# Performance work log

Measured on AMD Instinct MI355X. Metric: run time of the kernel, lower is better.

Reference implementation:

```python
import jax, jax.numpy as jnp
import numpy as np

N = 50000        # nodes
E = 800000       # edges
D_IN = 512       # input_shape
PROJ = 256       # proj_dim
H = 4            # num_heads
C = 32           # hidden_channels
HC = H * C
NUM_LABELS = 10
SLOPE = 0.2      # GATv2 LeakyReLU negative slope


def _glorot(key, shape):
    fan_in = shape[-1]
    return jax.random.normal(key, shape, jnp.float32) / jnp.sqrt(jnp.float32(fan_in))


def setup_inputs() -> dict:
    key = jax.random.key(0)
    ks = jax.random.split(key, 16)
    inp = {}
    inp["x"] = jax.random.normal(ks[0], (N, D_IN), jnp.float32)
    inp["edge_index"] = jax.random.randint(ks[1], (2, E), 0, N, dtype=jnp.int64)
    # projection Linear
    inp["W_proj"] = _glorot(ks[2], (PROJ, D_IN)); inp["b_proj"] = jnp.zeros((PROJ,), jnp.float32)
    # GATv2 layer 1: lin_l, lin_r, att, bias
    inp["Wl1"] = _glorot(ks[3], (HC, PROJ)); inp["bl1"] = jnp.zeros((HC,), jnp.float32)
    inp["Wr1"] = _glorot(ks[4], (HC, PROJ)); inp["br1"] = jnp.zeros((HC,), jnp.float32)
    inp["att1"] = _glorot(ks[5], (H, C)); inp["bias1"] = jnp.zeros((HC,), jnp.float32)
    # GATv2 layer 2
    inp["Wl2"] = _glorot(ks[6], (HC, HC)); inp["bl2"] = jnp.zeros((HC,), jnp.float32)
    inp["Wr2"] = _glorot(ks[7], (HC, HC)); inp["br2"] = jnp.zeros((HC,), jnp.float32)
    inp["att2"] = _glorot(ks[8], (H, C)); inp["bias2"] = jnp.zeros((HC,), jnp.float32)
    # head MLP
    inp["W1"] = _glorot(ks[9], (C, HC)); inp["b1"] = jnp.zeros((C,), jnp.float32)
    inp["W2"] = _glorot(ks[10], (NUM_LABELS, C)); inp["b2"] = jnp.zeros((NUM_LABELS,), jnp.float32)
    return inp


def _gatv2(x, src, dst, Wl, bl, Wr, br, att, bias):
    # x: [N, F_in]; src/dst: [E]. PyG GATv2Conv, concat=True, no self-loops, eval (no dropout).
    xl = (x @ Wl.T + bl).reshape(N, H, C)   # source transform
    xr = (x @ Wr.T + br).reshape(N, H, C)   # target transform
    e = jax.nn.leaky_relu(xl[src] + xr[dst], negative_slope=SLOPE)  # [E,H,C]
    logit = jnp.einsum('ehc,hc->eh', e, att)                        # [E,H]
    # segment softmax over incoming edges of each destination node
    m = jax.ops.segment_max(logit, dst, num_segments=N)             # [N,H]
    m = jnp.where(jnp.isfinite(m), m, jnp.float32(0))               # empty segments -> 0
    p = jnp.exp(logit - m[dst])                                     # [E,H]
    s = jax.ops.segment_sum(p, dst, num_segments=N)                 # [N,H]
    alpha = p / (s[dst] + jnp.float32(1e-16))                       # [E,H]
    out = jax.ops.segment_sum(xl[src] * alpha[:, :, None], dst, num_segments=N)  # [N,H,C]
    return out.reshape(N, HC) + bias


def reference(x, edge_index, W_proj, b_proj, Wl1, bl1, Wr1, br1, att1, bias1,
              Wl2, bl2, Wr2, br2, att2, bias2, W1, b1, W2, b2):
    src, dst = edge_index[0], edge_index[1]
    h = jax.nn.elu(x @ W_proj.T + b_proj)
    h = jax.nn.elu(_gatv2(h, src, dst, Wl1, bl1, Wr1, br1, att1, bias1))
    h = jax.nn.elu(_gatv2(h, src, dst, Wl2, bl2, Wr2, br2, att2, bias2))
    h = jax.nn.elu(h @ W1.T + b1)
    return h @ W2.T + b2
```

## Files before the change

kernel.cpp:

```cpp
#include <hip/hip_runtime.h>
#include <cstdint>
#include <cstddef>

constexpr int NN = 50000;
constexpr int NE = 800000;

typedef _Float16 half8 __attribute__((ext_vector_type(8)));
typedef _Float16 half4v __attribute__((ext_vector_type(4)));
typedef _Float16 half2v __attribute__((ext_vector_type(2)));
typedef float f32x16 __attribute__((ext_vector_type(16)));
typedef unsigned short ushort_t;

__device__ inline ushort_t f2h(float f) {
  _Float16 h = (_Float16)f;
  return __builtin_bit_cast(ushort_t, h);
}

#if __has_builtin(__builtin_amdgcn_fdot2)
__device__ inline float fdot2(half2v a, half2v b, float c) {
  return __builtin_amdgcn_fdot2(a, b, c, false);
}
#else
__device__ inline float fdot2(half2v a, half2v b, float c) {
  return c + (float)a[0] * (float)b[0] + (float)a[1] * (float)b[1];
}
#endif

__global__ void k_wconv(const float* __restrict__ W, ushort_t* __restrict__ Bh,
                        int M, int K, int total) {
  int idx = blockIdx.x * 256 + threadIdx.x;
  if (idx >= total) return;
  int j = idx & 7;
  int l = (idx >> 3) & 63;
  int blk = idx >> 9;
  int nKB = K >> 4;
  int cb = blk / nKB, kb = blk - cb * nKB;
  int col = cb * 32 + (l & 31);
  int k = kb * 16 + ((l >> 5) & 1) * 8 + j;
  float v = (col < M) ? W[(size_t)col * K + k] : 0.f;
  Bh[idx] = f2h(v);
}

__global__ __launch_bounds__(512) void gemm_proj_l1(const float* __restrict__ x,
    const ushort_t* __restrict__ WpF, const ushort_t* __restrict__ WB1,
    const float* __restrict__ bp, const float* __restrict__ bl1,
    const float* __restrict__ br1, ushort_t* __restrict__ xlh,
    ushort_t* __restrict__ xrh, int N)
{
  constexpr int NKK = 4;
  constexpr int nKB1 = 32;
  constexpr int nK1 = 8;
  __shared__ ushort_t Ah[2][2 * NKK * 512];
  __shared__ ushort_t H0[16384];
  const int t = threadIdx.x;
  const int lane = t & 63;
  const int wid = t >> 6;
  const int wr = wid >> 2;
  const int wc = wid & 3;
  const int row0 = blockIdx.x * 64;
  const int cb0 = wc * 2;

  const int s_r = t >> 4, s_k = (t & 15) * 4;
  const int sb0 = (s_k >> 4) * 512 + (s_r + 32 * ((s_k >> 3) & 1)) * 8 + (s_k & 7);
  const int sb1 = sb0 + NKK * 512;
  const bool ok0 = (row0 + s_r) < N;
  const bool ok1 = (row0 + s_r + 32) < N;
  const float* ap0 = x + (size_t)(row0 + s_r) * 512 + s_k;
  const float* ap1 = x + (size_t)(row0 + s_r + 32) * 512 + s_k;

  f32x16 acc0 = {}, acc1 = {};
  float4 f0 = make_float4(0, 0, 0, 0), f1 = make_float4(0, 0, 0, 0);

  auto aload = [&](int ks) {
    f0 = make_float4(0, 0, 0, 0);
    f1 = make_float4(0, 0, 0, 0);
    if (ok0) f0 = *(const float4*)(ap0 + (size_t)ks * 64);
    if (ok1) f1 = *(const float4*)(ap1 + (size_t)ks * 64);
  };
  auto cvt4 = [](float4 f) {
    half4v h;
    h[0] = (_Float16)f.x; h[1] = (_Float16)f.y;
    h[2] = (_Float16)f.z; h[3] = (_Float16)f.w;
    return h;
  };
  auto stage_write = [&](int buf) {
    *(half4v*)&Ah[buf][sb0] = cvt4(f0);
    *(half4v*)&Ah[buf][sb1] = cvt4(f1);
  };

  aload(0);
  stage_write(0);
  __syncthreads();

  for (int ks = 0; ks < nK1; ++ks) {
    const int cur = ks & 1;
    const int nxt = cur ^ 1;
    const bool have_next = (ks + 1 < nK1);
    if (have_next) aload(ks + 1);

    #pragma unroll
    for (int kk = 0; kk < NKK; ++kk) {
      const int kbg = ks * NKK + kk;
      half8 ah = *(const half8*)&Ah[cur][(wr * NKK + kk) * 512 + lane * 8];
      const size_t bo0 = ((size_t)(cb0 * nKB1 + kbg) * 64 + lane) * 8;
      half8 bh0 = *(const half8*)(WpF + bo0);
      acc0 = __builtin_amdgcn_mfma_f32_32x32x16_f16(ah, bh0, acc0, 0, 0, 0);
      const size_t bo1 = ((size_t)((cb0 + 1) * nKB1 + kbg) * 64 + lane) * 8;
      half8 bh1 = *(const half8*)(WpF + bo1);
      acc1 = __builtin_amdgcn_mfma_f32_32x32x16_f16(ah, bh1, acc1, 0, 0, 0);
    }

    if (have_next) stage_write(nxt);
    __syncthreads();
  }

  {
    int col = cb0 * 32 + (lane & 31);
    float bv = bp[col];
    #pragma unroll
    for (int r = 0; r < 16; ++r) {
      int row = wr * 32 + (r & 3) + 8 * (r >> 2) + 4 * (lane >> 5);
      float v = acc0[r] + bv;
      v = v > 0.f ? v : (__expf(v) - 1.f);
      H0[((row >> 5) * 16 + (col >> 4)) * 512 +
         ((row & 31) + 32 * ((col >> 3) & 1)) * 8 + (col & 7)] = f2h(v);
    }
    int col1 = col + 32;
    float bv1 = bp[col1];
    #pragma unroll
    for (int r = 0; r < 16; ++r) {
      int row = wr * 32 + (r & 3) + 8 * (r >> 2) + 4 * (lane >> 5);
      float v = acc1[r] + bv1;
      v = v > 0.f ? v : (__expf(v) - 1.f);
      H0[((row >> 5) * 16 + (col1 >> 4)) * 512 +
         ((row & 31) + 32 * ((col1 >> 3) & 1)) * 8 + (col1 & 7)] = f2h(v);
    }
  }
  __syncthreads();

  f32x16 acc2a = {}, acc2b = {};
  #pragma unroll
  for (int kk = 0; kk < 16; ++kk) {
    half8 ah = *(const half8*)&H0[(wr * 16 + kk) * 512 + lane * 8];
    const size_t bo0 = ((size_t)(cb0 * 16 + kk) * 64 + lane) * 8;
    half8 bh0 = *(const half8*)(WB1 + bo0);
    acc2a = __builtin_amdgcn_mfma_f32_32x32x16_f16(ah, bh0, acc2a, 0, 0, 0);
    const size_t bo1 = ((size_t)((cb0 + 1) * 16 + kk) * 64 + lane) * 8;
    half8 bh1 = *(const half8*)(WB1 + bo1);
    acc2b = __builtin_amdgcn_mfma_f32_32x32x16_f16(ah, bh1, acc2b, 0, 0, 0);
  }

  auto epi2 = [&](const f32x16& acc, int cb) {
    int cc = cb * 32 + (lane & 31);
    float bv = (cc < 128) ? bl1[cc] : br1[cc - 128];
    #pragma unroll
    for (int r = 0; r < 16; ++r) {
      int rr = row0 + wr * 32 + (r & 3) + 8 * (r >> 2) + 4 * (lane >> 5);
      if (rr < N) {
        float v = acc[r] + bv;
        if (cc < 128) xlh[(size_t)rr * 128 + cc] = f2h(v);
        else          xrh[(size_t)rr * 128 + (cc - 128)] = f2h(v);
      }
    }
  };
  epi2(acc2a, cb0);
  epi2(acc2b, cb0 + 1);
}

template<int ACT, int OUTMODE, int BKT, int AFP16, int NCB>
__global__ __launch_bounds__(512) void gemm_mfma(const void* __restrict__ Av,
    const ushort_t* __restrict__ Bh,
    const float* __restrict__ bias, const float* __restrict__ bias2,
    float* __restrict__ C, ushort_t* __restrict__ C16a,
    ushort_t* __restrict__ C16b, int N, int M, int K)
{
  constexpr int NKK = BKT / 16;
  __shared__ ushort_t Ah[2][2 * NKK * 512];
  const int t = threadIdx.x;
  const int lane = t & 63;
  const int wid = t >> 6;
  const int wr = wid >> 2;
  const int wc = wid & 3;
  const int row0 = blockIdx.x * 64;
  const int col0 = blockIdx.y * (128 * NCB);
  const int nKB = K >> 4;
  const int nK = K / BKT;
  const int cb0 = (col0 >> 5) + wc * NCB;

  int s_r, s_k, sb0, sb1 = 0;
  bool ok0 = false, ok1 = false;
  if constexpr (!AFP16) {
    s_r = t >> 4; s_k = (t & 15) * 4;
    sb0 = (s_k >> 4) * 512 + (s_r + 32 * ((s_k >> 3) & 1)) * 8 + (s_k & 7);
    sb1 = sb0 + NKK * 512;
    ok0 = (row0 + s_r) < N;
    ok1 = (row0 + s_r + 32) < N;
  } else if constexpr (BKT == 64) {
    s_r = t >> 3; s_k = (t & 7) * 8;
    sb0 = ((s_r >> 5) * NKK + (s_k >> 4)) * 512 +
          ((s_r & 31) + 32 * ((s_k >> 3) & 1)) * 8;
    ok0 = (row0 + s_r) < N;
  } else {
    s_r = t >> 3; s_k = (t & 7) * 4;
    sb0 = ((s_r >> 5) * NKK + (s_k >> 4)) * 512 +
          ((s_r & 31) + 32 * ((s_k >> 3) & 1)) * 8 + (s_k & 7);
    ok0 = (row0 + s_r) < N;
  }
  const float*    ap0 = (const float*)Av + (size_t)(row0 + s_r) * K + s_k;
  const float*    ap1 = (const float*)Av + (size_t)(row0 + s_r + 32) * K + s_k;
  const ushort_t* aph = (const ushort_t*)Av + (size_t)(row0 + s_r) * K + s_k;

  f32x16 acc0 = {}, acc1 = {};
  float4 f0 = make_float4(0, 0, 0, 0), f1 = make_float4(0, 0, 0, 0);
  half8 h8 = {};
  half4v h4 = {};

  auto aload = [&](int ks) {
    if constexpr (!AFP16) {
      f0 = make_float4(0, 0, 0, 0);
      f1 = make_float4(0, 0, 0, 0);
      if (ok0) f0 = *(const float4*)(ap0 + (size_t)ks * BKT);
      if (ok1) f1 = *(const float4*)(ap1 + (size_t)ks * BKT);
    } else if constexpr (BKT == 64) {
      half8 z = {};
      h8 = ok0 ? *(const half8*)(aph + (size_t)ks * BKT) : z;
    } else {
      half4v z = {};
      h4 = ok0 ? *(const half4v*)(aph + (size_t)ks * BKT) : z;
    }
  };
  auto cvt4 = [](float4 f) {
    half4v h;
    h[0] = (_Float16)f.x; h[1] = (_Float16)f.y;
    h[2] = (_Float16)f.z; h[3] = (_Float16)f.w;
    return h;
  };
  auto stage_write = [&](int buf) {
    if constexpr (!AFP16) {
      *(half4v*)&Ah[buf][sb0] = cvt4(f0);
      *(half4v*)&Ah[buf][sb1] = cvt4(f1);
    } else if constexpr (BKT == 64) {
      *(half8*)&Ah[buf][sb0] = h8;
    } else {
      *(half4v*)&Ah[buf][sb0] = h4;
    }
  };

  aload(0);
  stage_write(0);
  __syncthreads();

  for (int ks = 0; ks < nK; ++ks) {
    const int cur = ks & 1;
    const int nxt = cur ^ 1;
    const bool have_next = (ks + 1 < nK);
    if (have_next) aload(ks + 1);

    #pragma unroll
    for (int kk = 0; kk < NKK; ++kk) {
      const int kbg = ks * NKK + kk;
      half8 ah = *(const half8*)&Ah[cur][(wr * NKK + kk) * 512 + lane * 8];
      const size_t bo0 = ((size_t)(cb0 * nKB + kbg) * 64 + lane) * 8;
      half8 bh0 = *(const half8*)(Bh + bo0);
      acc0 = __builtin_amdgcn_mfma_f32_32x32x16_f16(ah, bh0, acc0, 0, 0, 0);
      if constexpr (NCB == 2) {
        const size_t bo1 = ((size_t)((cb0 + 1) * nKB + kbg) * 64 + lane) * 8;
        half8 bh1 = *(const half8*)(Bh + bo1);
        acc1 = __builtin_amdgcn_mfma_f32_32x32x16_f16(ah, bh1, acc1, 0, 0, 0);
      }
    }

    if (have_next) stage_write(nxt);
    __syncthreads();
  }

  auto epi = [&](const f32x16& acc, int cb) {
    int cc = cb * 32 + (lane & 31);
    float bv;
    if constexpr (OUTMODE == 3) bv = (cc < 128) ? bias[cc] : bias2[cc - 128];
    else                        bv = (cc < M) ? bias[cc] : 0.f;
    #pragma unroll
    for (int r = 0; r < 16; ++r) {
      int rr = row0 + wr * 32 + (r & 3) + 8 * (r >> 2) + 4 * (lane >> 5);
      if (rr < N && cc < M) {
        float v = acc[r] + bv;
        if (ACT) v = v > 0.f ? v : (__expf(v) - 1.f);
        if constexpr (OUTMODE == 0)      C[(size_t)rr * M + cc] = v;
        else if constexpr (OUTMODE == 1) C16a[(size_t)rr * M + cc] = f2h(v);
        else {
          if (cc < 128) C16a[(size_t)rr * 128 + cc] = f2h(v);
          else          C16b[(size_t)rr * 128 + (cc - 128)] = f2h(v);
        }
      }
    }
  };
  epi(acc0, cb0);
  if constexpr (NCB == 2) epi(acc1, cb0 + 1);
}

__global__ void k_degrank(const int* __restrict__ ei, int* __restrict__ deg,
                          int* __restrict__ rank) {
  int e = blockIdx.x * 256 + threadIdx.x;
  if (e >= NE) return;
  int d = ei[NE + e];
  rank[e] = atomicAdd(&deg[d], 1);
}

__global__ __launch_bounds__(256) void k_scan1(const int* __restrict__ deg,
    int* __restrict__ rowstart, int* __restrict__ blocksum) {
  __shared__ int sm[256];
  int b = blockIdx.x, t = threadIdx.x;
  int i = b * 256 + t;
  int v = (i < NN) ? deg[i] : 0;
  sm[t] = v;
  __syncthreads();
  #pragma unroll
  for (int off = 1; off < 256; off <<= 1) {
    int u = (t >= off) ? sm[t - off] : 0;
    __syncthreads();
    sm[t] += u;
    __syncthreads();
  }
  if (i < NN) rowstart[i + 1] = sm[t];
  if (t == 255) blocksum[b] = sm[255];
}

__global__ __launch_bounds__(256) void k_scan2(int* __restrict__ blocksum, int nb) {
  __shared__ int sm[256];
  int t = threadIdx.x;
  int v = (t < nb) ? blocksum[t] : 0;
  sm[t] = v;
  __syncthreads();
  #pragma unroll
  for (int off = 1; off < 256; off <<= 1) {
    int u = (t >= off) ? sm[t - off] : 0;
    __syncthreads();
    sm[t] += u;
    __syncthreads();
  }
  if (t < nb) blocksum[t] = (t == 0) ? 0 : sm[t - 1];
}

__global__ __launch_bounds__(256) void k_scan3(int* __restrict__ rowstart,
    const int* __restrict__ blocksum) {
  int b = blockIdx.x, t = threadIdx.x;
  int i = b * 256 + t;
  if (i == 0) rowstart[0] = 0;
  if (i < NN) rowstart[i + 1] += blocksum[b];
}

__global__ void k_scatter(const int* __restrict__ ei, const int* __restrict__ rowstart,
                          const int* __restrict__ rank, int* __restrict__ srcp) {
  int e = blockIdx.x * 256 + threadIdx.x;
  if (e >= NE) return;
  int d = ei[NE + e];
  srcp[rowstart[d] + rank[e]] = ei[e];
}

__global__ __launch_bounds__(256) void k_gat(const ushort_t* __restrict__ xl,
    const ushort_t* __restrict__ xr, const int* __restrict__ srcp,
    const int* __restrict__ rowstart, const float* __restrict__ att,
    const float* __restrict__ bias, ushort_t* __restrict__ out)
{
  const int g = threadIdx.x >> 5;
  const int c = threadIdx.x & 31;
  const int n = blockIdx.x * 8 + g;
  const int r0 = rowstart[n], r1 = rowstart[n + 1];
  half4v xrh = *(const half4v*)(xr + (size_t)n * 128 + 4 * c);
  const half2v xr01 = {xrh[0], xrh[1]};
  const half2v xr23 = {xrh[2], xrh[3]};
  const float4 atv = *(const float4*)(att + 4 * c);
  const half2v at01 = {(_Float16)atv.x, (_Float16)atv.y};
  const half2v at23 = {(_Float16)atv.z, (_Float16)atv.w};
  const half2v k02 = {(_Float16)0.2f, (_Float16)0.2f};

  float m = -1e30f, ssum = 0.f;
  float a0 = 0.f, a1 = 0.f, a2 = 0.f, a3 = 0.f;

  auto lg = [&](int s, float4& xs) -> float {
    half4v hv = *(const half4v*)(xl + (size_t)s * 128 + 4 * c);
    xs.x = (float)hv[0]; xs.y = (float)hv[1];
    xs.z = (float)hv[2]; xs.w = (float)hv[3];
    half2v u01 = half2v{hv[0], hv[1]} + xr01;
    half2v u23 = half2v{hv[2], hv[3]} + xr23;
    u01 = __builtin_elementwise_max(u01, u01 * k02);
    u23 = __builtin_elementwise_max(u23, u23 * k02);
    float l = fdot2(u01, at01, fdot2(u23, at23, 0.f));
    l += __shfl_xor(l, 1);
    l += __shfl_xor(l, 2);
    l += __shfl_xor(l, 4);
    return l;
  };

  int j = r0;
  for (; j + 8 <= r1; j += 8) {
    int s0 = srcp[j],     s1 = srcp[j + 1], s2 = srcp[j + 2], s3 = srcp[j + 3];
    int s4 = srcp[j + 4], s5 = srcp[j + 5], s6 = srcp[j + 6], s7 = srcp[j + 7];
    float4 x0, x1, x2, x3, x4, x5, x6, x7;
    float l0 = lg(s0, x0), l1 = lg(s1, x1), l2 = lg(s2, x2), l3 = lg(s3, x3);
    float l4 = lg(s4, x4), l5 = lg(s5, x5), l6 = lg(s6, x6), l7 = lg(s7, x7);
    float mloc = fmaxf(fmaxf(fmaxf(l0, l1), fmaxf(l2, l3)),
                       fmaxf(fmaxf(l4, l5), fmaxf(l6, l7)));
    float mn = fmaxf(m, mloc);
    float sc = __expf(m - mn);
    float p0 = __expf(l0 - mn), p1 = __expf(l1 - mn);
    float p2 = __expf(l2 - mn), p3 = __expf(l3 - mn);
    float p4 = __expf(l4 - mn), p5 = __expf(l5 - mn);
    float p6 = __expf(l6 - mn), p7 = __expf(l7 - mn);
    ssum = ssum * sc + (((p0 + p1) + (p2 + p3)) + ((p4 + p5) + (p6 + p7)));
    a0 = a0 * sc + (((p0 * x0.x + p1 * x1.x) + (p2 * x2.x + p3 * x3.x)) +
                    ((p4 * x4.x + p5 * x5.x) + (p6 * x6.x + p7 * x7.x)));
    a1 = a1 * sc + (((p0 * x0.y + p1 * x1.y) + (p2 * x2.y + p3 * x3.y)) +
                    ((p4 * x4.y + p5 * x5.y) + (p6 * x6.y + p7 * x7.y)));
    a2 = a2 * sc + (((p0 * x0.z + p1 * x1.z) + (p2 * x2.z + p3 * x3.z)) +
                    ((p4 * x4.z + p5 * x5.z) + (p6 * x6.z + p7 * x7.z)));
    a3 = a3 * sc + (((p0 * x0.w + p1 * x1.w) + (p2 * x2.w + p3 * x3.w)) +
                    ((p4 * x4.w + p5 * x5.w) + (p6 * x6.w + p7 * x7.w)));
    m = mn;
  }
  for (; j + 4 <= r1; j += 4) {
    int s0 = srcp[j], s1 = srcp[j + 1], s2 = srcp[j + 2], s3 = srcp[j + 3];
    float4 x0, x1, x2, x3;
    float l0 = lg(s0, x0), l1 = lg(s1, x1), l2 = lg(s2, x2), l3 = lg(s3, x3);
    float mloc = fmaxf(fmaxf(l0, l1), fmaxf(l2, l3));
    float mn = fmaxf(m, mloc);
    float sc = __expf(m - mn);
    float p0 = __expf(l0 - mn), p1 = __expf(l1 - mn);
    float p2 = __expf(l2 - mn), p3 = __expf(l3 - mn);
    ssum = ssum * sc + ((p0 + p1) + (p2 + p3));
    a0 = a0 * sc + (p0 * x0.x + p1 * x1.x) + (p2 * x2.x + p3 * x3.x);
    a1 = a1 * sc + (p0 * x0.y + p1 * x1.y) + (p2 * x2.y + p3 * x3.y);
    a2 = a2 * sc + (p0 * x0.z + p1 * x1.z) + (p2 * x2.z + p3 * x3.z);
    a3 = a3 * sc + (p0 * x0.w + p1 * x1.w) + (p2 * x2.w + p3 * x3.w);
    m = mn;
  }
  for (; j < r1; ++j) {
    float4 xs;
    float l = lg(srcp[j], xs);
    float mn = fmaxf(m, l);
    float sc = __expf(m - mn);
    float p = __expf(l - mn);
    ssum = ssum * sc + p;
    a0 = a0 * sc + p * xs.x;
    a1 = a1 * sc + p * xs.y;
    a2 = a2 * sc + p * xs.z;
    a3 = a3 * sc + p * xs.w;
    m = mn;
  }

  const float4 bv = *(const float4*)(bias + 4 * c);
  float rinv = 1.f / (ssum + 1e-16f);
  float o0 = a0 * rinv + bv.x;
  float o1 = a1 * rinv + bv.y;
  float o2 = a2 * rinv + bv.z;
  float o3 = a3 * rinv + bv.w;
  o0 = o0 > 0.f ? o0 : (__expf(o0) - 1.f);
  o1 = o1 > 0.f ? o1 : (__expf(o1) - 1.f);
  o2 = o2 > 0.f ? o2 : (__expf(o2) - 1.f);
  o3 = o3 > 0.f ? o3 : (__expf(o3) - 1.f);
  half4v ov;
  ov[0] = (_Float16)o0; ov[1] = (_Float16)o1;
  ov[2] = (_Float16)o2; ov[3] = (_Float16)o3;
  *(half4v*)(out + (size_t)n * 128 + 4 * c) = ov;
}

__global__ void k_report_ws(float* out, int out_size, float wsz) {
  int i = blockIdx.x * 256 + threadIdx.x;
  if (i < out_size) out[i] = (i == 0) ? wsz : 0.f;
}

extern "C" void kernel_launch(void* const* d_in, const int* in_sizes, int n_in,
                              void* d_out, int out_size, void* d_ws, size_t ws_size,
                              hipStream_t stream)
{
  const float* x    = (const float*)d_in[0];
  const int*   ei   = (const int*)d_in[1];
  const float* Wp   = (const float*)d_in[2];  const float* bp    = (const float*)d_in[3];
  const float* Wl1  = (const float*)d_in[4];  const float* bl1   = (const float*)d_in[5];
  const float* Wr1  = (const float*)d_in[6];  const float* br1   = (const float*)d_in[7];
  const float* att1 = (const float*)d_in[8];  const float* bias1 = (const float*)d_in[9];
  const float* Wl2  = (const float*)d_in[10]; const float* bl2   = (const float*)d_in[11];
  const float* Wr2  = (const float*)d_in[12]; const float* br2   = (const float*)d_in[13];
  const float* att2 = (const float*)d_in[14]; const float* bias2 = (const float*)d_in[15];
  const float* W1   = (const float*)d_in[16]; const float* b1    = (const float*)d_in[17];
  const float* W2   = (const float*)d_in[18]; const float* b2    = (const float*)d_in[19];
  float* out = (float*)d_out;

  constexpr size_t NEED = 122300000;
  if (ws_size < NEED) {
    k_report_ws<<<(out_size + 255) / 256, 256, 0, stream>>>(out, out_size, (float)ws_size);
    return;
  }
  char* ws = (char*)d_ws;
  ushort_t* h1h   = (ushort_t*)(ws + 0);
  ushort_t* h2h   = (ushort_t*)(ws + 25600000);
  ushort_t* xlh   = (ushort_t*)(ws + 51200000);
  ushort_t* xrh   = (ushort_t*)(ws + 76800000);
  ushort_t* h3h   = (ushort_t*)(ws + 102400000);
  ushort_t* wb    = (ushort_t*)(ws + 108800000);
  int*      srcp  = (int*)(ws + 115200000);
  int*      rank  = (int*)(ws + 118400000);
  int*      deg   = (int*)(ws + 121600000);
  int*      rowst = (int*)(ws + 122000000);
  int*      bsum  = (int*)(ws + 122250000);

  ushort_t* Wph  = wb;
  ushort_t* WB1h = wb + 131072;
  ushort_t* WB2h = wb + 196608;
  ushort_t* W1h  = wb + 229376;
  ushort_t* W2h  = wb + 233472;

  hipMemsetAsync(deg, 0, NN * sizeof(int), stream);

  k_wconv<<<(131072+255)/256, 256, 0, stream>>>(Wp,  Wph,          256, 512, 131072);
  k_wconv<<<(32768+255)/256,  256, 0, stream>>>(Wl1, WB1h,         128, 256, 32768);
  k_wconv<<<(32768+255)/256,  256, 0, stream>>>(Wr1, WB1h + 32768, 128, 256, 32768);
  k_wconv<<<(16384+255)/256,  256, 0, stream>>>(Wl2, WB2h,         128, 128, 16384);
  k_wconv<<<(16384+255)/256,  256, 0, stream>>>(Wr2, WB2h + 16384, 128, 128, 16384);
  k_wconv<<<(4096+255)/256,   256, 0, stream>>>(W1,  W1h,          32,  128, 4096);
  k_wconv<<<(1024+255)/256,   256, 0, stream>>>(W2,  W2h,          10,  32,  1024);

  constexpr int NB = (NN + 255) / 256;
  k_degrank<<<(NE+255)/256, 256, 0, stream>>>(ei, deg, rank);
  k_scan1  <<<NB, 256, 0, stream>>>(deg, rowst, bsum);
  k_scan2  <<<1, 256, 0, stream>>>(bsum, NB);
  k_scan3  <<<NB, 256, 0, stream>>>(rowst, bsum);
  k_scatter<<<(NE+255)/256, 256, 0, stream>>>(ei, rowst, rank, srcp);

  constexpr int GX = (NN + 63) / 64;

  gemm_proj_l1<<<GX, 512, 0, stream>>>(x, Wph, WB1h, bp, bl1, br1, xlh, xrh, NN);
  k_gat<<<NN/8, 256, 0, stream>>>(xlh, xrh, srcp, rowst, att1, bias1, h1h);

  gemm_mfma<0,3,64,1,2><<<dim3(GX, 1), 512, 0, stream>>>(
      h1h, WB2h, bl2, br2, nullptr, xlh, xrh, NN, 256, 128);
  k_gat<<<NN/8, 256, 0, stream>>>(xlh, xrh, srcp, rowst, att2, bias2, h2h);

  gemm_mfma<1,1,64,1,1><<<dim3(GX, 1), 512, 0, stream>>>(
      h2h, W1h, b1, nullptr, nullptr, h3h, nullptr, NN, 32, 128);
  gemm_mfma<0,0,32,1,1><<<dim3(GX, 1), 512, 0, stream>>>(
      h3h, W2h, b2, nullptr, out, nullptr, nullptr, NN, 10, 32);
}
```

Measured before the change: 255.9 us.

## Fuse head MLP GEMMs into one kernel and unify GAT edge loop tails

Replaces the two separate head GEMM launches with one kernel that computes the 128->32 layer with ELU, stages the fp16 result in shared memory, and immediately applies the 32->10 layer. This removes the global round trip through h3 and one kernel launch. The GAT aggregation loop also drops its 4-wide and scalar tail loops, handling tails in the 8-wide loop with clamped source indices and masked logits. The masked lanes do redundant gathers, and in the fused kernel only one of four wave columns does MFMA work.

```diff
diff --git a/kernel.cpp b/kernel.cpp
--- a/kernel.cpp
+++ b/kernel.cpp
@@ -165,6 +165,92 @@
   };
   epi2(acc2a, cb0);
   epi2(acc2b, cb0 + 1);
+}
+
+__global__ __launch_bounds__(512) void gemm_mlp(const ushort_t* __restrict__ h2,
+    const ushort_t* __restrict__ W1F, const ushort_t* __restrict__ W2F,
+    const float* __restrict__ b1, const float* __restrict__ b2,
+    float* __restrict__ out, int N)
+{
+  constexpr int NKK = 4;
+  __shared__ ushort_t Ah[2][2 * NKK * 512];
+  __shared__ ushort_t H3[2048];
+  const int t = threadIdx.x;
+  const int lane = t & 63;
+  const int wid = t >> 6;
+  const int wr = wid >> 2;
+  const int wc = wid & 3;
+  const int row0 = blockIdx.x * 64;
+
+  const int s_r = t >> 3, s_k = (t & 7) * 8;
+  const int sb0 = ((s_r >> 5) * NKK + (s_k >> 4)) * 512 +
+                  ((s_r & 31) + 32 * ((s_k >> 3) & 1)) * 8;
+  const bool ok0 = (row0 + s_r) < N;
+  const ushort_t* aph = h2 + (size_t)(row0 + s_r) * 128 + s_k;
+
+  f32x16 acc = {};
+  half8 h8 = {};
+
+  auto aload = [&](int ks) {
+    half8 z = {};
+    h8 = ok0 ? *(const half8*)(aph + (size_t)ks * 64) : z;
+  };
+
+  aload(0);
+  *(half8*)&Ah[0][sb0] = h8;
+  __syncthreads();
+
+  for (int ks = 0; ks < 2; ++ks) {
+    const int cur = ks & 1;
+    const bool have_next = (ks == 0);
+    if (have_next) aload(1);
+
+    if (wc == 0) {
+      #pragma unroll
+      for (int kk = 0; kk < NKK; ++kk) {
+        const int kbg = ks * NKK + kk;
+        half8 ah = *(const half8*)&Ah[cur][(wr * NKK + kk) * 512 + lane * 8];
+        half8 bh = *(const half8*)(W1F + ((size_t)kbg * 64 + lane) * 8);
+        acc = __builtin_amdgcn_mfma_f32_32x32x16_f16(ah, bh, acc, 0, 0, 0);
+      }
+    }
+
+    if (have_next) *(half8*)&Ah[cur ^ 1][sb0] = h8;
+    __syncthreads();
+  }
+
+  if (wc == 0) {
+    int cc = lane & 31;
+    float bv = b1[cc];
+    #pragma unroll
+    for (int r = 0; r < 16; ++r) {
+      int row = wr * 32 + (r & 3) + 8 * (r >> 2) + 4 * (lane >> 5);
+      float v = acc[r] + bv;
+      v = v > 0.f ? v : (__expf(v) - 1.f);
+      H3[((row >> 5) * 2 + (cc >> 4)) * 512 +
+         ((row & 31) + 32 * ((cc >> 3) & 1)) * 8 + (cc & 7)] = f2h(v);
+    }
+  }
+  __syncthreads();
+
+  if (wc == 0) {
+    f32x16 acc2 = {};
+    #pragma unroll
+    for (int kk = 0; kk < 2; ++kk) {
+      half8 ah = *(const half8*)&H3[(wr * 2 + kk) * 512 + lane * 8];
+      half8 bh = *(const half8*)(W2F + ((size_t)kk * 64 + lane) * 8);
+      acc2 = __builtin_amdgcn_mfma_f32_32x32x16_f16(ah, bh, acc2, 0, 0, 0);
+    }
+    int cc = lane & 31;
+    if (cc < 10) {
+      float bv = b2[cc];
+      #pragma unroll
+      for (int r = 0; r < 16; ++r) {
+        int rr = row0 + wr * 32 + (r & 3) + 8 * (r >> 2) + 4 * (lane >> 5);
+        if (rr < N) out[(size_t)rr * 10 + cc] = acc2[r] + bv;
+      }
+    }
+  }
 }
 
 template<int ACT, int OUTMODE, int BKT, int AFP16, int NCB>
@@ -392,13 +478,23 @@
     return l;
   };
 
-  int j = r0;
-  for (; j + 8 <= r1; j += 8) {
-    int s0 = srcp[j],     s1 = srcp[j + 1], s2 = srcp[j + 2], s3 = srcp[j + 3];
-    int s4 = srcp[j + 4], s5 = srcp[j + 5], s6 = srcp[j + 6], s7 = srcp[j + 7];
+  const int je = r1 - 1;
+  for (int j = r0; j < r1; j += 8) {
+    int s0 = srcp[j];
+    int s1 = srcp[min(j + 1, je)], s2 = srcp[min(j + 2, je)];
+    int s3 = srcp[min(j + 3, je)], s4 = srcp[min(j + 4, je)];
+    int s5 = srcp[min(j + 5, je)], s6 = srcp[min(j + 6, je)];
+    int s7 = srcp[min(j + 7, je)];
     float4 x0, x1, x2, x3, x4, x5, x6, x7;
     float l0 = lg(s0, x0), l1 = lg(s1, x1), l2 = lg(s2, x2), l3 = lg(s3, x3);
     float l4 = lg(s4, x4), l5 = lg(s5, x5), l6 = lg(s6, x6), l7 = lg(s7, x7);
+    l1 = (j + 1 < r1) ? l1 : -1e30f;
+    l2 = (j + 2 < r1) ? l2 : -1e30f;
+    l3 = (j + 3 < r1) ? l3 : -1e30f;
+    l4 = (j + 4 < r1) ? l4 : -1e30f;
+    l5 = (j + 5 < r1) ? l5 : -1e30f;
+    l6 = (j + 6 < r1) ? l6 : -1e30f;
+    l7 = (j + 7 < r1) ? l7 : -1e30f;
     float mloc = fmaxf(fmaxf(fmaxf(l0, l1), fmaxf(l2, l3)),
                        fmaxf(fmaxf(l4, l5), fmaxf(l6, l7)));
     float mn = fmaxf(m, mloc);
@@ -418,35 +514,6 @@
                     ((p4 * x4.w + p5 * x5.w) + (p6 * x6.w + p7 * x7.w)));
     m = mn;
   }
-  for (; j + 4 <= r1; j += 4) {
-    int s0 = srcp[j], s1 = srcp[j + 1], s2 = srcp[j + 2], s3 = srcp[j + 3];
-    float4 x0, x1, x2, x3;
-    float l0 = lg(s0, x0), l1 = lg(s1, x1), l2 = lg(s2, x2), l3 = lg(s3, x3);
-    float mloc = fmaxf(fmaxf(l0, l1), fmaxf(l2, l3));
-    float mn = fmaxf(m, mloc);
-    float sc = __expf(m - mn);
-    float p0 = __expf(l0 - mn), p1 = __expf(l1 - mn);
-    float p2 = __expf(l2 - mn), p3 = __expf(l3 - mn);
-    ssum = ssum * sc + ((p0 + p1) + (p2 + p3));
-    a0 = a0 * sc + (p0 * x0.x + p1 * x1.x) + (p2 * x2.x + p3 * x3.x);
-    a1 = a1 * sc + (p0 * x0.y + p1 * x1.y) + (p2 * x2.y + p3 * x3.y);
-    a2 = a2 * sc + (p0 * x0.z + p1 * x1.z) + (p2 * x2.z + p3 * x3.z);
-    a3 = a3 * sc + (p0 * x0.w + p1 * x1.w) + (p2 * x2.w + p3 * x3.w);
-    m = mn;
-  }
-  for (; j < r1; ++j) {
-    float4 xs;
-    float l = lg(srcp[j], xs);
-    float mn = fmaxf(m, l);
-    float sc = __expf(m - mn);
-    float p = __expf(l - mn);
-    ssum = ssum * sc + p;
-    a0 = a0 * sc + p * xs.x;
-    a1 = a1 * sc + p * xs.y;
-    a2 = a2 * sc + p * xs.z;
-    a3 = a3 * sc + p * xs.w;
-    m = mn;
-  }
 
   const float4 bv = *(const float4*)(bias + 4 * c);
   float rinv = 1.f / (ssum + 1e-16f);
@@ -496,7 +563,6 @@
   ushort_t* h2h   = (ushort_t*)(ws + 25600000);
   ushort_t* xlh   = (ushort_t*)(ws + 51200000);
   ushort_t* xrh   = (ushort_t*)(ws + 76800000);
-  ushort_t* h3h   = (ushort_t*)(ws + 102400000);
   ushort_t* wb    = (ushort_t*)(ws + 108800000);
   int*      srcp  = (int*)(ws + 115200000);
   int*      rank  = (int*)(ws + 118400000);
@@ -536,8 +602,5 @@
       h1h, WB2h, bl2, br2, nullptr, xlh, xrh, NN, 256, 128);
   k_gat<<<NN/8, 256, 0, stream>>>(xlh, xrh, srcp, rowst, att2, bias2, h2h);
 
-  gemm_mfma<1,1,64,1,1><<<dim3(GX, 1), 512, 0, stream>>>(
-      h2h, W1h, b1, nullptr, nullptr, h3h, nullptr, NN, 32, 128);
-  gemm_mfma<0,0,32,1,1><<<dim3(GX, 1), 512, 0, stream>>>(
-      h3h, W2h, b2, nullptr, out, nullptr, nullptr, NN, 10, 32);
-}
+  gemm_mlp<<<GX, 512, 0, stream>>>(h2h, W1h, W2h, b1, b2, out, NN);
+}
```

Result: faster. 240.7 us (-5.9%).
